# Performance work log

Measured on AMD Instinct MI355X. Metric: run time of the kernel, lower is better.

Reference implementation:

```python
import jax, jax.numpy as jnp
import numpy as np

T, N, I, H, OUT = 16, 4096, 4, 32, 1


def setup_inputs() -> dict:
    key = jax.random.key(0)
    ks = jax.random.split(key, 12)
    f32 = jnp.float32
    x_path = jax.random.normal(ks[0], (T, N, I), f32)
    adj = jax.random.normal(ks[1], (N, N), f32) / np.float32(np.sqrt(N))
    W_enc = jax.random.normal(ks[2], (I, H), f32) / np.float32(np.sqrt(I))
    b_enc = jnp.zeros((H,), f32)
    W_gcn = jax.random.normal(ks[3], (H, H), f32) / np.float32(np.sqrt(H))
    b_gcn = jnp.zeros((H,), f32)
    W_time = jax.random.normal(ks[4], (H, H), f32) / np.float32(np.sqrt(H))
    b_time = jnp.zeros((H,), f32)
    W_proj = jax.random.normal(ks[5], (H, H * I), f32) * np.float32(0.1 / np.sqrt(H))
    b_proj = jnp.zeros((H * I,), f32)
    W_d1 = jax.random.normal(ks[6], (H, 16), f32) / np.float32(np.sqrt(H))
    b_d1 = jnp.zeros((16,), f32)
    W_d2 = jax.random.normal(ks[7], (16, OUT), f32) / np.float32(4.0)
    b_d2 = jnp.zeros((OUT,), f32)
    return dict(x_path=x_path, adj=adj, W_enc=W_enc, b_enc=b_enc,
                W_gcn=W_gcn, b_gcn=b_gcn, W_time=W_time, b_time=b_time,
                W_proj=W_proj, b_proj=b_proj, W_d1=W_d1, b_d1=b_d1,
                W_d2=W_d2, b_d2=b_d2)


def _natural_cubic_coeffs(y):
    # y: (T, C) samples on uniform grid t=0..T-1 (h=1).
    # Natural cubic spline: tridiagonal solve for second derivatives M.
    Tn = y.shape[0]
    main = jnp.ones((Tn,), y.dtype).at[1:-1].set(4.0)
    A = jnp.diag(main)
    idx = jnp.arange(1, Tn - 1)
    A = A.at[idx, idx - 1].set(1.0).at[idx, idx + 1].set(1.0)
    rhs = jnp.zeros_like(y).at[1:-1].set(6.0 * (y[2:] - 2.0 * y[1:-1] + y[:-2]))
    M = jnp.linalg.solve(A, rhs)
    b = (y[1:] - y[:-1]) - (2.0 * M[:-1] + M[1:]) / 6.0
    c = M[:-1] / 2.0
    d = (M[1:] - M[:-1]) / 6.0
    return b, c, d  # each (T-1, C); dX/dt on interval i at local s: b+2cs+3ds^2


def reference(x_path, adj, W_enc, b_enc, W_gcn, b_gcn, W_time, b_time,
              W_proj, b_proj, W_d1, b_d1, W_d2, b_d2):
    Tn, Nn, In = x_path.shape
    Hn = W_enc.shape[1]
    y = x_path.reshape(Tn, Nn * In)
    sb, sc, sd = _natural_cubic_coeffs(y)

    # z0 = encoder(X(t0)); spline value at grid point 0 equals the sample.
    z0 = x_path[0] @ W_enc + b_enc  # (N, H)

    def vf(z, dxdt):
        # SpatialVectorField + projector + block-diagonal Jacobian applied to dX/dt.
        # z: (N, H), dxdt: (N, I)
        zn = adj @ z                                     # GCN neighbor aggregation
        h = jax.nn.relu(zn @ W_gcn + b_gcn + z @ W_time + b_time)
        sens = (h @ W_proj + b_proj).reshape(Nn, Hn, In)  # per-site Jacobian blocks
        # site_identity * sens -> block-diag; matmul with dX reduces to per-site contraction
        return jnp.einsum('nhi,ni->nh', sens, dxdt)

    def rk4_step(z, coefs):
        bi, ci, di = coefs  # (N*I,)
        def dxdt(s):
            return (bi + 2.0 * ci * s + 3.0 * di * s * s).reshape(Nn, In)
        k1 = vf(z, dxdt(0.0))
        k2 = vf(z + 0.5 * k1, dxdt(0.5))
        k3 = vf(z + 0.5 * k2, dxdt(0.5))
        k4 = vf(z + k3, dxdt(1.0))
        zn = z + (k1 + 2.0 * k2 + 2.0 * k3 + k4) / 6.0
        return zn, zn

    _, zs = jax.lax.scan(rk4_step, z0, (sb, sc, sd))
    zT = jnp.concatenate([z0[None], zs], axis=0)  # (T, N, H)

    hdec = jax.nn.relu(zT @ W_d1 + b_d1)
    return jax.nn.sigmoid(hdec @ W_d2 + b_d2)  # (T, N, OUT)
```

## Files before the change

### kernel.cpp

```cpp
#include <hip/hip_runtime.h>
#include <hip/hip_bf16.h>

#define NN 4096
#define NI 16384
#define HH 32

typedef __attribute__((ext_vector_type(8))) short short8;
typedef __attribute__((ext_vector_type(4))) float f32x4;
typedef unsigned long long u64;

union bfrag { short8 s8; u64 q[2]; };

__device__ __forceinline__ short f2bs(float f) {
  __hip_bfloat16 b = __float2bfloat16(f);
  return *(short*)&b;
}

__device__ __forceinline__ unsigned pack2(float lo, float hi) {
  return (unsigned)(unsigned short)f2bs(lo) |
         ((unsigned)(unsigned short)f2bs(hi) << 16);
}

__device__ __forceinline__ long zt_idx(int n, int h) {
  const int hb = h >> 4, hl = h & 15;
  const int kb = n >> 5, oct = (n >> 3) & 3, j = n & 7;
  return ((long)(hb * 128 + kb) * 64 + hl + 16 * oct) * 8 + j;
}

__global__ void k_spline(const float* __restrict__ x,
                         float* __restrict__ dx0, float* __restrict__ dxh,
                         float* __restrict__ dx1, unsigned* __restrict__ bar) {
  if (blockIdx.x == 0) {
    for (int i = threadIdx.x; i < 576; i += 256) bar[i] = 0u;
  }
  const int c = blockIdx.x * 256 + threadIdx.x;
  float y[16];
#pragma unroll
  for (int t = 0; t < 16; ++t) y[t] = x[t * NI + c];
  float cp[15], dp[15], M[16];
  cp[1] = 0.25f;
  dp[1] = (6.f * (y[2] - 2.f * y[1] + y[0])) * 0.25f;
#pragma unroll
  for (int i = 2; i <= 14; ++i) {
    float ri = 6.f * (y[i + 1] - 2.f * y[i] + y[i - 1]);
    float inv = 1.f / (4.f - cp[i - 1]);
    cp[i] = inv;
    dp[i] = (ri - dp[i - 1]) * inv;
  }
  M[0] = 0.f; M[15] = 0.f;
  M[14] = dp[14];
#pragma unroll
  for (int i = 13; i >= 1; --i) M[i] = dp[i] - cp[i] * M[i + 1];
#pragma unroll
  for (int i = 0; i < 15; ++i) {
    float b = (y[i + 1] - y[i]) - (2.f * M[i] + M[i + 1]) * (1.f / 6.f);
    float cc = 0.5f * M[i];
    float dd = (M[i + 1] - M[i]) * (1.f / 6.f);
    dx0[i * NI + c] = b;
    dxh[i * NI + c] = b + cc + 0.75f * dd;
    dx1[i * NI + c] = b + 2.f * cc + 3.f * dd;
  }
}

__device__ __forceinline__ void dec_block(const float* zsrc ,
                                          const float* Wd1s ,
                                          const float* dsm, float* op,
                                          int r0, int tid) {
  if (tid < 256) {
    const int rr = tid >> 4, jj = tid & 15;
    float hv = dsm[jj];
#pragma unroll
    for (int hh = 0; hh < 32; ++hh) hv = fmaf(zsrc[rr * 33 + hh], Wd1s[hh * 16 + jj], hv);
    float val = fmaxf(hv, 0.f) * dsm[16 + jj];
#pragma unroll
    for (int off = 1; off < 16; off <<= 1) val += __shfl_xor(val, off, 64);
    if (jj == 0)
      __hip_atomic_store(op + r0 + rr, 1.f / (1.f + expf(-(dsm[32] + val))),
                         __ATOMIC_RELAXED, __HIP_MEMORY_SCOPE_AGENT);
  }
}

__global__ __launch_bounds__(1024, 4) void k_ode(
    const float* __restrict__ adj, const float* __restrict__ x,
    const float* __restrict__ dx0, const float* __restrict__ dxh,
    const float* __restrict__ dx1,
    const float* __restrict__ We, const float* __restrict__ be,
    const float* __restrict__ Wg, const float* __restrict__ bg,
    const float* __restrict__ Wt, const float* __restrict__ bt,
    const float* __restrict__ Wp, const float* __restrict__ bp,
    const float* __restrict__ Wd1, const float* __restrict__ bd1,
    const float* __restrict__ Wd2, const float* __restrict__ bd2,
    short* __restrict__ zTa, short* __restrict__ zTb,
    unsigned* __restrict__ bar, float* __restrict__ out) {
  __shared__ float red2[16][34][17];
  __shared__ float zn_s[16][33];
  __shared__ float h_s[16][33];
  __shared__ float ze_s[16][33];
  __shared__ float zb_s[16][33];
  __shared__ float ka_s[16][33];
  __shared__ float Wg_s[32][32];
  __shared__ float Wt_s[32][32];
  __shared__ float Wp_s[32][136];
  __shared__ float Wd1_s[32][16];
  __shared__ float bgt_s[32];
  __shared__ float bp_s[128];
  __shared__ float dsm[33];

  const int tid = threadIdx.x;
  const int lane = tid & 63;
  const int w = tid >> 6;
  const int bid = blockIdx.x;
  const int r0 = bid * 16;
  const int fr = lane & 15, oct = lane >> 4;
  unsigned* cnt_mine = bar + (bid >> 4) * 32;
  unsigned* cnt_wave = bar + w * 32;

  short8 av[8];
  {
    const float* arow = adj + (long)(r0 + fr) * NN + w * 256 + oct * 8;
#pragma unroll
    for (int i = 0; i < 8; ++i) {
      const float4 u0 = *(const float4*)(arow + i * 32);
      const float4 u1 = *(const float4*)(arow + i * 32 + 4);
      short8 rf;
      rf[0] = f2bs(u0.x); rf[1] = f2bs(u0.y); rf[2] = f2bs(u0.z); rf[3] = f2bs(u0.w);
      rf[4] = f2bs(u1.x); rf[5] = f2bs(u1.y); rf[6] = f2bs(u1.z); rf[7] = f2bs(u1.w);
      av[i] = rf;
    }
  }

  Wg_s[tid >> 5][tid & 31] = Wg[tid];
  Wt_s[tid >> 5][tid & 31] = Wt[tid];
#pragma unroll
  for (int idx = tid; idx < 4096; idx += 1024)
    Wp_s[idx >> 7][idx & 127] = Wp[idx];
  if (tid < 512) Wd1_s[tid >> 4][tid & 15] = Wd1[tid];
  if (tid < 32) bgt_s[tid] = bg[tid] + bt[tid];
  if (tid < 128) bp_s[tid] = bp[tid];
  if (tid < 16) { dsm[tid] = bd1[tid]; dsm[16 + tid] = Wd2[tid]; }
  if (tid == 0) dsm[32] = bd2[0];

  const int r = (tid >> 5) & 15, c = tid & 31;
  if (tid < 512) {
    const int n = r0 + r;
    float acc = be[c];
#pragma unroll
    for (int i = 0; i < 4; ++i) acc = fmaf(x[n * 4 + i], We[i * 32 + c], acc);
    zb_s[r][c] = acc;
    ze_s[r][c] = acc;
  }
  __syncthreads();

  if (w == 6) {
    const int q = tid - 384, cc = q & 31, rr = (q >> 5) * 8;
    const u64 pk0 = (u64)pack2(ze_s[rr][cc], ze_s[rr + 1][cc]) |
                    ((u64)pack2(ze_s[rr + 2][cc], ze_s[rr + 3][cc]) << 32);
    const u64 pk1 = (u64)pack2(ze_s[rr + 4][cc], ze_s[rr + 5][cc]) |
                    ((u64)pack2(ze_s[rr + 6][cc], ze_s[rr + 7][cc]) << 32);
    __hip_atomic_store((u64*)zTa + (zt_idx(r0 + rr, cc) >> 2), pk0,
                       __ATOMIC_RELAXED, __HIP_MEMORY_SCOPE_AGENT);
    __hip_atomic_store((u64*)zTa + (zt_idx(r0 + rr + 4, cc) >> 2), pk1,
                       __ATOMIC_RELAXED, __HIP_MEMORY_SCOPE_AGENT);
    if (lane == 0) {
      asm volatile("s_waitcnt vmcnt(0)" ::: "memory");
      __hip_atomic_fetch_add(cnt_mine, 1u, __ATOMIC_RELAXED, __HIP_MEMORY_SCOPE_AGENT);
    }
  }
  dec_block(&zb_s[0][0], &Wd1_s[0][0], dsm, out, r0, tid);

  for (int e = 1; e <= 60; ++e) {
    const int tt = (e - 1) >> 2, j = ((e - 1) & 3) + 1;
    const float* dxp = (j == 1) ? dx0 + tt * NI
                     : (j == 4) ? dx1 + tt * NI : dxh + tt * NI;
    const short* zi = (e & 1) ? zTa : zTb;
    short* zo = (e & 1) ? zTb : zTa;

    float4 dxv;
    if (tid < 512) dxv = *(const float4*)(dxp + (long)(r0 + r) * 4);

    unsigned cv = 0;
    if (lane == 0) {
      cv = __hip_atomic_load(cnt_wave, __ATOMIC_RELAXED, __HIP_MEMORY_SCOPE_AGENT);
      while (cv < (unsigned)(16 * e)) {
        __builtin_amdgcn_s_sleep(1);
        cv = __hip_atomic_load(cnt_wave, __ATOMIC_RELAXED, __HIP_MEMORY_SCOPE_AGENT);
      }
    }
    cv = (unsigned)__builtin_amdgcn_readfirstlane((int)cv);

    f32x4 a0 = {0.f, 0.f, 0.f, 0.f}, a1 = {0.f, 0.f, 0.f, 0.f};
    const u64* bq = (const u64*)zi + (size_t)w * 1024 + (lane << 1) + (cv >> 31);
    bfrag bf[8];
#pragma unroll
    for (int i = 0; i < 8; ++i) {
      bf[i].q[0] = __hip_atomic_load(bq + i * 128,
                                     __ATOMIC_RELAXED, __HIP_MEMORY_SCOPE_AGENT);
      bf[i].q[1] = __hip_atomic_load(bq + i * 128 + 1,
                                     __ATOMIC_RELAXED, __HIP_MEMORY_SCOPE_AGENT);
    }
#pragma unroll
    for (int i = 0; i < 8; ++i)
      a0 = __builtin_amdgcn_mfma_f32_16x16x32_bf16(av[i], bf[i].s8, a0, 0, 0, 0);
#pragma unroll
    for (int i = 0; i < 8; ++i) {
      bf[i].q[0] = __hip_atomic_load(bq + 16384 + i * 128,
                                     __ATOMIC_RELAXED, __HIP_MEMORY_SCOPE_AGENT);
      bf[i].q[1] = __hip_atomic_load(bq + 16384 + i * 128 + 1,
                                     __ATOMIC_RELAXED, __HIP_MEMORY_SCOPE_AGENT);
    }
#pragma unroll
    for (int i = 0; i < 8; ++i)
      a1 = __builtin_amdgcn_mfma_f32_16x16x32_bf16(av[i], bf[i].s8, a1, 0, 0, 0);

    {
      const int crow = (lane >> 4) * 4, ccol = lane & 15;
#pragma unroll
      for (int q = 0; q < 4; ++q) {
        red2[crow + q][ccol][w] = a0[q];
        red2[crow + q][ccol + 16][w] = a1[q];
      }
    }
    __syncthreads();

    if (tid < 512) {
      float zn = 0.f;
#pragma unroll
      for (int q = 0; q < 16; ++q) zn += red2[r][c][q];
      zn_s[r][c] = zn;
    }
    __syncthreads();

    if (tid < 512) {
      float hv = bgt_s[c];
#pragma unroll
      for (int kk = 0; kk < 32; ++kk)
        hv = fmaf(zn_s[r][kk], Wg_s[kk][c], fmaf(ze_s[r][kk], Wt_s[kk][c], hv));
      h_s[r][c] = fmaxf(hv, 0.f);
    }
    __syncthreads();

    if (tid < 512) {
      float s0 = bp_s[c * 4], s1 = bp_s[c * 4 + 1];
      float s2 = bp_s[c * 4 + 2], s3 = bp_s[c * 4 + 3];
#pragma unroll
      for (int hp = 0; hp < 32; ++hp) {
        const float4 wv = *(const float4*)&Wp_s[hp][c * 4];
        const float hr = h_s[r][hp];
        s0 = fmaf(hr, wv.x, s0);
        s1 = fmaf(hr, wv.y, s1);
        s2 = fmaf(hr, wv.z, s2);
        s3 = fmaf(hr, wv.w, s3);
      }
      const float kv = s0 * dxv.x + s1 * dxv.y + s2 * dxv.z + s3 * dxv.w;
      float zev;
      if (j == 1)      { ka_s[r][c] = kv;            zev = zb_s[r][c] + 0.5f * kv; }
      else if (j == 2) { ka_s[r][c] += 2.f * kv;     zev = zb_s[r][c] + 0.5f * kv; }
      else if (j == 3) { ka_s[r][c] += 2.f * kv;     zev = zb_s[r][c] + kv; }
      else { zev = zb_s[r][c] + (ka_s[r][c] + kv) * (1.f / 6.f); zb_s[r][c] = zev; }
      ze_s[r][c] = zev;
    }
    __syncthreads();

    if (w == 6) {
      const int q = tid - 384, cc = q & 31, rr = (q >> 5) * 8;
      const u64 pk0 = (u64)pack2(ze_s[rr][cc], ze_s[rr + 1][cc]) |
                      ((u64)pack2(ze_s[rr + 2][cc], ze_s[rr + 3][cc]) << 32);
      const u64 pk1 = (u64)pack2(ze_s[rr + 4][cc], ze_s[rr + 5][cc]) |
                      ((u64)pack2(ze_s[rr + 6][cc], ze_s[rr + 7][cc]) << 32);
      __hip_atomic_store((u64*)zo + (zt_idx(r0 + rr, cc) >> 2), pk0,
                         __ATOMIC_RELAXED, __HIP_MEMORY_SCOPE_AGENT);
      __hip_atomic_store((u64*)zo + (zt_idx(r0 + rr + 4, cc) >> 2), pk1,
                         __ATOMIC_RELAXED, __HIP_MEMORY_SCOPE_AGENT);
      if (lane == 0) {
        asm volatile("s_waitcnt vmcnt(0)" ::: "memory");
        __hip_atomic_fetch_add(cnt_mine, 1u, __ATOMIC_RELAXED, __HIP_MEMORY_SCOPE_AGENT);
      }
    }
    if (j == 4)
      dec_block(&zb_s[0][0], &Wd1_s[0][0], dsm, out + (tt + 1) * NN, r0, tid);
  }
}

extern "C" void kernel_launch(void* const* d_in, const int* in_sizes, int n_in,
                              void* d_out, int out_size, void* d_ws, size_t ws_size,
                              hipStream_t stream) {
  (void)in_sizes; (void)n_in; (void)out_size; (void)ws_size;
  const float* x      = (const float*)d_in[0];
  const float* adj    = (const float*)d_in[1];
  const float* W_enc  = (const float*)d_in[2];
  const float* b_enc  = (const float*)d_in[3];
  const float* W_gcn  = (const float*)d_in[4];
  const float* b_gcn  = (const float*)d_in[5];
  const float* W_time = (const float*)d_in[6];
  const float* b_time = (const float*)d_in[7];
  const float* W_proj = (const float*)d_in[8];
  const float* b_proj = (const float*)d_in[9];
  const float* W_d1   = (const float*)d_in[10];
  const float* b_d1   = (const float*)d_in[11];
  const float* W_d2   = (const float*)d_in[12];
  const float* b_d2   = (const float*)d_in[13];
  float* out = (float*)d_out;

  float* dx0 = (float*)d_ws;
  float* dxh = dx0 + 15 * NI;
  float* dx1 = dxh + 15 * NI;
  short* zTa = (short*)(dx1 + 15 * NI);
  short* zTb = zTa + HH * NN;
  unsigned* bar = (unsigned*)(zTb + HH * NN);

  k_spline<<<64, 256, 0, stream>>>(x, dx0, dxh, dx1, bar);

  void* args[] = {(void*)&adj, (void*)&x, (void*)&dx0, (void*)&dxh, (void*)&dx1,
                  (void*)&W_enc, (void*)&b_enc, (void*)&W_gcn, (void*)&b_gcn,
                  (void*)&W_time, (void*)&b_time, (void*)&W_proj, (void*)&b_proj,
                  (void*)&W_d1, (void*)&b_d1, (void*)&W_d2, (void*)&b_d2,
                  (void*)&zTa, (void*)&zTb, (void*)&bar, (void*)&out};
  hipError_t err = hipLaunchCooperativeKernel((const void*)k_ode, dim3(256),
                                              dim3(1024), args, 0, stream);
  if (err != hipSuccess) {
    k_ode<<<256, 1024, 0, stream>>>(adj, x, dx0, dxh, dx1, W_enc, b_enc,
                                    W_gcn, b_gcn, W_time, b_time, W_proj, b_proj,
                                    W_d1, b_d1, W_d2, b_d2, zTa, zTb, bar, out);
  }
}
```

Measured before the change: 784.9 us.

## Publish z state per wave without extra barrier and overlap decoder with reduction

Each of the eight compute waves now packs and publishes its own two rows of the updated state straight after the RK update, instead of a single wave doing it after an extra __syncthreads. The grid-barrier wait threshold is raised to count per-wave arrivals. The decoder for the previous timestep is moved into idle threads during the reduction phase, taking it off the critical path, with the final timestep decoded after the loop. The cooperative launch is replaced by a plain launch, which relies on all 256 blocks being co-resident for the spin barrier to avoid deadlock.

```diff
diff --git a/kernel.cpp b/kernel.cpp
--- a/kernel.cpp
+++ b/kernel.cpp
@@ -62,22 +62,20 @@
   }
 }
 
-__device__ __forceinline__ void dec_block(const float* zsrc ,
-                                          const float* Wd1s ,
-                                          const float* dsm, float* op,
-                                          int r0, int tid) {
-  if (tid < 256) {
-    const int rr = tid >> 4, jj = tid & 15;
-    float hv = dsm[jj];
-#pragma unroll
-    for (int hh = 0; hh < 32; ++hh) hv = fmaf(zsrc[rr * 33 + hh], Wd1s[hh * 16 + jj], hv);
-    float val = fmaxf(hv, 0.f) * dsm[16 + jj];
-#pragma unroll
-    for (int off = 1; off < 16; off <<= 1) val += __shfl_xor(val, off, 64);
-    if (jj == 0)
-      __hip_atomic_store(op + r0 + rr, 1.f / (1.f + expf(-(dsm[32] + val))),
-                         __ATOMIC_RELAXED, __HIP_MEMORY_SCOPE_AGENT);
-  }
+__device__ __forceinline__ void dec_rows(const float* zsrc ,
+                                         const float* Wd1s ,
+                                         const float* dsm, float* op,
+                                         int r0, int q) {
+  const int rr = q >> 4, jj = q & 15;
+  float hv = dsm[jj];
+#pragma unroll
+  for (int hh = 0; hh < 32; ++hh) hv = fmaf(zsrc[rr * 33 + hh], Wd1s[hh * 16 + jj], hv);
+  float val = fmaxf(hv, 0.f) * dsm[16 + jj];
+#pragma unroll
+  for (int off = 1; off < 16; off <<= 1) val += __shfl_xor(val, off, 64);
+  if (jj == 0)
+    __hip_atomic_store(op + r0 + rr, 1.f / (1.f + expf(-(dsm[32] + val))),
+                       __ATOMIC_RELAXED, __HIP_MEMORY_SCOPE_AGENT);
 }
 
 __global__ __launch_bounds__(1024, 4) void k_ode(
@@ -141,6 +139,7 @@
   if (tid == 0) dsm[32] = bd2[0];
 
   const int r = (tid >> 5) & 15, c = tid & 31;
+  float zenc = 0.f;
   if (tid < 512) {
     const int n = r0 + r;
     float acc = be[c];
@@ -148,25 +147,22 @@
     for (int i = 0; i < 4; ++i) acc = fmaf(x[n * 4 + i], We[i * 32 + c], acc);
     zb_s[r][c] = acc;
     ze_s[r][c] = acc;
+    zenc = acc;
   }
   __syncthreads();
 
-  if (w == 6) {
-    const int q = tid - 384, cc = q & 31, rr = (q >> 5) * 8;
-    const u64 pk0 = (u64)pack2(ze_s[rr][cc], ze_s[rr + 1][cc]) |
-                    ((u64)pack2(ze_s[rr + 2][cc], ze_s[rr + 3][cc]) << 32);
-    const u64 pk1 = (u64)pack2(ze_s[rr + 4][cc], ze_s[rr + 5][cc]) |
-                    ((u64)pack2(ze_s[rr + 6][cc], ze_s[rr + 7][cc]) << 32);
-    __hip_atomic_store((u64*)zTa + (zt_idx(r0 + rr, cc) >> 2), pk0,
-                       __ATOMIC_RELAXED, __HIP_MEMORY_SCOPE_AGENT);
-    __hip_atomic_store((u64*)zTa + (zt_idx(r0 + rr + 4, cc) >> 2), pk1,
-                       __ATOMIC_RELAXED, __HIP_MEMORY_SCOPE_AGENT);
+  if (tid < 512) {
+    const float zhi = __shfl_down(zenc, 32);
+    if (lane < 32)
+      __hip_atomic_store((unsigned*)zTa + (zt_idx(r0 + 2 * w, lane) >> 1),
+                         pack2(zenc, zhi),
+                         __ATOMIC_RELAXED, __HIP_MEMORY_SCOPE_AGENT);
     if (lane == 0) {
       asm volatile("s_waitcnt vmcnt(0)" ::: "memory");
       __hip_atomic_fetch_add(cnt_mine, 1u, __ATOMIC_RELAXED, __HIP_MEMORY_SCOPE_AGENT);
     }
   }
-  dec_block(&zb_s[0][0], &Wd1_s[0][0], dsm, out, r0, tid);
+  if (tid < 256) dec_rows(&zb_s[0][0], &Wd1_s[0][0], dsm, out, r0, tid);
 
   for (int e = 1; e <= 60; ++e) {
     const int tt = (e - 1) >> 2, j = ((e - 1) & 3) + 1;
@@ -181,7 +177,7 @@
     unsigned cv = 0;
     if (lane == 0) {
       cv = __hip_atomic_load(cnt_wave, __ATOMIC_RELAXED, __HIP_MEMORY_SCOPE_AGENT);
-      while (cv < (unsigned)(16 * e)) {
+      while (cv < (unsigned)(128 * e)) {
         __builtin_amdgcn_s_sleep(1);
         cv = __hip_atomic_load(cnt_wave, __ATOMIC_RELAXED, __HIP_MEMORY_SCOPE_AGENT);
       }
@@ -227,6 +223,8 @@
 #pragma unroll
       for (int q = 0; q < 16; ++q) zn += red2[r][c][q];
       zn_s[r][c] = zn;
+    } else if (j == 1 && e > 1 && tid < 768) {
+      dec_rows(&zb_s[0][0], &Wd1_s[0][0], dsm, out + tt * NN, r0, tid - 512);
     }
     __syncthreads();
 
@@ -258,27 +256,21 @@
       else if (j == 3) { ka_s[r][c] += 2.f * kv;     zev = zb_s[r][c] + kv; }
       else { zev = zb_s[r][c] + (ka_s[r][c] + kv) * (1.f / 6.f); zb_s[r][c] = zev; }
       ze_s[r][c] = zev;
-    }
-    __syncthreads();
-
-    if (w == 6) {
-      const int q = tid - 384, cc = q & 31, rr = (q >> 5) * 8;
-      const u64 pk0 = (u64)pack2(ze_s[rr][cc], ze_s[rr + 1][cc]) |
-                      ((u64)pack2(ze_s[rr + 2][cc], ze_s[rr + 3][cc]) << 32);
-      const u64 pk1 = (u64)pack2(ze_s[rr + 4][cc], ze_s[rr + 5][cc]) |
-                      ((u64)pack2(ze_s[rr + 6][cc], ze_s[rr + 7][cc]) << 32);
-      __hip_atomic_store((u64*)zo + (zt_idx(r0 + rr, cc) >> 2), pk0,
-                         __ATOMIC_RELAXED, __HIP_MEMORY_SCOPE_AGENT);
-      __hip_atomic_store((u64*)zo + (zt_idx(r0 + rr + 4, cc) >> 2), pk1,
-                         __ATOMIC_RELAXED, __HIP_MEMORY_SCOPE_AGENT);
+
+      const float zhi = __shfl_down(zev, 32);
+      if (lane < 32)
+        __hip_atomic_store((unsigned*)zo + (zt_idx(r0 + 2 * w, lane) >> 1),
+                           pack2(zev, zhi),
+                           __ATOMIC_RELAXED, __HIP_MEMORY_SCOPE_AGENT);
       if (lane == 0) {
         asm volatile("s_waitcnt vmcnt(0)" ::: "memory");
         __hip_atomic_fetch_add(cnt_mine, 1u, __ATOMIC_RELAXED, __HIP_MEMORY_SCOPE_AGENT);
       }
     }
-    if (j == 4)
-      dec_block(&zb_s[0][0], &Wd1_s[0][0], dsm, out + (tt + 1) * NN, r0, tid);
-  }
+  }
+
+  __syncthreads();
+  if (tid < 256) dec_rows(&zb_s[0][0], &Wd1_s[0][0], dsm, out + 15 * NN, r0, tid);
 }
 
 extern "C" void kernel_launch(void* const* d_in, const int* in_sizes, int n_in,
@@ -310,16 +302,7 @@
 
   k_spline<<<64, 256, 0, stream>>>(x, dx0, dxh, dx1, bar);
 
-  void* args[] = {(void*)&adj, (void*)&x, (void*)&dx0, (void*)&dxh, (void*)&dx1,
-                  (void*)&W_enc, (void*)&b_enc, (void*)&W_gcn, (void*)&b_gcn,
-                  (void*)&W_time, (void*)&b_time, (void*)&W_proj, (void*)&b_proj,
-                  (void*)&W_d1, (void*)&b_d1, (void*)&W_d2, (void*)&b_d2,
-                  (void*)&zTa, (void*)&zTb, (void*)&bar, (void*)&out};
-  hipError_t err = hipLaunchCooperativeKernel((const void*)k_ode, dim3(256),
-                                              dim3(1024), args, 0, stream);
-  if (err != hipSuccess) {
-    k_ode<<<256, 1024, 0, stream>>>(adj, x, dx0, dxh, dx1, W_enc, b_enc,
-                                    W_gcn, b_gcn, W_time, b_time, W_proj, b_proj,
-                                    W_d1, b_d1, W_d2, b_d2, zTa, zTb, bar, out);
-  }
-}
+  k_ode<<<256, 1024, 0, stream>>>(adj, x, dx0, dxh, dx1, W_enc, b_enc,
+                                  W_gcn, b_gcn, W_time, b_time, W_proj, b_proj,
+                                  W_d1, b_d1, W_d2, b_d2, zTa, zTb, bar, out);
+}
```

Result: slower. 1.109 ms (+41.3%).
